# Kernel tuning notes

Hardware: AMD Instinct MI355X
Metric: run time of the kernel (lower is better)

## Reference

```python
import jax, jax.numpy as jnp
import numpy as np

B, T, HID = 2, 2048, 2048
H, DQ, DV, R = 16, 128, 128, 32
DCQ, DCKV, DCO = 768, 512, 512
EPS = 1e-6
SCALE = DQ ** -0.5


def _rms(x, w):
    xf = x.astype(jnp.float32)
    var = jnp.mean(xf * xf, axis=-1, keepdims=True)
    return w * (xf * jax.lax.rsqrt(var + EPS)).astype(x.dtype)


def _rotate_half(x):
    d = x.shape[-1] // 2
    return jnp.concatenate([-x[..., d:], x[..., :d]], axis=-1)


def setup_inputs() -> dict:
    key = jax.random.key(0)
    ks = jax.random.split(key, 9)
    s = 0.02
    hidden_states = jax.random.normal(ks[0], (B, T, HID), dtype=jnp.float32)
    # RoPE tables: inv_freq over R/2 dims, duplicated (cat(freqs, freqs))
    inv_freq = 1.0 / (10000.0 ** (np.arange(0, R, 2, dtype=np.float32) / R))
    freqs = np.arange(T, dtype=np.float32)[:, None] * inv_freq[None, :]  # [T, R/2]
    emb = np.concatenate([freqs, freqs], axis=-1)  # [T, R]
    cos = jnp.asarray(np.cos(emb))
    sin = jnp.asarray(np.sin(emb))
    return {
        "hidden_states": hidden_states,
        "cos": cos,
        "sin": sin,
        "Wq_shared": jax.random.normal(ks[1], (DCQ, HID), jnp.float32) * s,
        "q_shared_norm_w": jnp.ones((DCQ,), jnp.float32),
        "Wkv_shared": jax.random.normal(ks[2], (DCKV, HID), jnp.float32) * s,
        "kv_shared_norm_w": jnp.ones((DCKV,), jnp.float32),
        "Wq_private": jax.random.normal(ks[3], (H * DQ, DCQ), jnp.float32) * s,
        "Wkv_private": jax.random.normal(ks[4], (H * (DQ + DV), DCKV), jnp.float32) * s,
        "Wg_private": jax.random.normal(ks[5], (H * DV, HID), jnp.float32) * s,
        "Wo_private": jax.random.normal(ks[6], (DCO, H * DV), jnp.float32) * s,
        "o_private_norm_w": jnp.ones((DCO,), jnp.float32),
        "Wo_shared": jax.random.normal(ks[7], (HID, DCO), jnp.float32) * s,
    }


def reference(hidden_states, cos, sin, Wq_shared, q_shared_norm_w, Wkv_shared,
              kv_shared_norm_w, Wq_private, Wkv_private, Wg_private,
              Wo_private, o_private_norm_w, Wo_shared):
    x = hidden_states
    b, t, _ = x.shape
    # shared (latent) projections + RMSNorm
    q_shared = _rms(x @ Wq_shared.T, q_shared_norm_w)    # [B,T,DCQ]
    kv_shared = _rms(x @ Wkv_shared.T, kv_shared_norm_w)  # [B,T,DCKV]
    # private per-head projections
    q = (q_shared @ Wq_private.T).reshape(b, t, H, DQ).transpose(0, 2, 1, 3)
    kv = kv_shared @ Wkv_private.T                        # [B,T,H*(DQ+DV)]
    k_flat, v_flat = jnp.split(kv, 2, axis=-1)            # keys block then values block
    gates = jax.nn.silu(x @ Wg_private.T)                 # [B,T,H*DV]
    v_flat = v_flat * gates
    k = k_flat.reshape(b, t, H, DQ).transpose(0, 2, 1, 3)
    v = v_flat.reshape(b, t, H, DV).transpose(0, 2, 1, 3)
    # partial RoPE on first R dims of each head
    c = cos[None, None]  # [1,1,T,R]
    s = sin[None, None]
    q_rope, q_pass = q[..., :R], q[..., R:]
    k_rope, k_pass = k[..., :R], k[..., R:]
    q = jnp.concatenate([q_rope * c + _rotate_half(q_rope) * s, q_pass], axis=-1)
    k = jnp.concatenate([k_rope * c + _rotate_half(k_rope) * s, k_pass], axis=-1)
    # causal attention
    scores = jnp.einsum('bhqd,bhkd->bhqk', q, k) * SCALE
    causal = jnp.tril(jnp.ones((t, t), dtype=bool))
    scores = jnp.where(causal, scores, jnp.finfo(scores.dtype).min)
    attn = jax.nn.softmax(scores, axis=-1)
    out = jnp.einsum('bhqk,bhkd->bhqd', attn, v)
    out = out.transpose(0, 2, 1, 3).reshape(b, t, H * DV)
    # output subspace: private proj -> norm -> shared proj
    out = _rms(out @ Wo_private.T, o_private_norm_w)
    return out @ Wo_shared.T
```

## Files before the change

### kernel.cpp

```cpp
#include <hip/hip_runtime.h>
#include <stdint.h>

typedef __attribute__((ext_vector_type(8))) short short8;
typedef __attribute__((ext_vector_type(4))) short sh4;
typedef __attribute__((ext_vector_type(4))) float f32x4;

__device__ __forceinline__ float bf2f(unsigned short u) {
  union { unsigned int i; float f; } v; v.i = ((unsigned int)u) << 16; return v.f;
}
__device__ __forceinline__ unsigned short f2bf(float f) {
  union { float f; unsigned int i; } v; v.f = f;
  unsigned int u = v.i;
  return (unsigned short)((u + 0x7fffu + ((u >> 16) & 1u)) >> 16);
}

#define B_SZ 2
#define T_SEQ 2048
#define NH 16
#define DH 128
#define ROPE_R 32
#define SCALE_Q 0.08838834764831845f

template <bool F>
__device__ __forceinline__ short8 ld8(const void* base, size_t idx) {
  if constexpr (F) {
    const float* p = (const float*)base + idx;
    f32x4 a = *(const f32x4*)p;
    f32x4 b = *(const f32x4*)(p + 4);
    short8 r;
    r[0] = (short)f2bf(a[0]); r[1] = (short)f2bf(a[1]);
    r[2] = (short)f2bf(a[2]); r[3] = (short)f2bf(a[3]);
    r[4] = (short)f2bf(b[0]); r[5] = (short)f2bf(b[1]);
    r[6] = (short)f2bf(b[2]); r[7] = (short)f2bf(b[3]);
    return r;
  } else {
    return *(const short8*)((const unsigned short*)base + idx);
  }
}

template <bool AF, bool BF, bool C32>
__global__ __launch_bounds__(256) void gemm_bt(
    const void* __restrict__ Ap, const void* __restrict__ Bp,
    void* __restrict__ Cp, int M, int N, int K) {
  __shared__ unsigned short Al[128][40];
  __shared__ unsigned short Bl[128][40];
  const int tid = threadIdx.x;
  const int lane = tid & 63, w = tid >> 6;
  const int wm = w >> 1, wn = w & 1;
  const int quad = lane >> 4, l16 = lane & 15;
  const int m0 = blockIdx.y * 128, n0 = blockIdx.x * 128;
  f32x4 acc[4][4];
#pragma unroll
  for (int i = 0; i < 4; ++i)
#pragma unroll
    for (int j = 0; j < 4; ++j)
#pragma unroll
      for (int r = 0; r < 4; ++r) acc[i][j][r] = 0.f;

  for (int k0 = 0; k0 < K; k0 += 32) {
    __syncthreads();
#pragma unroll
    for (int p = 0; p < 2; ++p) {
      int v = tid + p * 256;
      int row = v >> 2, kc = (v & 3) * 8;
      *(short8*)&Al[row][kc] = ld8<AF>(Ap, (size_t)(m0 + row) * K + k0 + kc);
      *(short8*)&Bl[row][kc] = ld8<BF>(Bp, (size_t)(n0 + row) * K + k0 + kc);
    }
    __syncthreads();
    short8 a[4];
#pragma unroll
    for (int i = 0; i < 4; ++i)
      a[i] = *(const short8*)&Al[wm * 64 + i * 16 + l16][quad * 8];
#pragma unroll
    for (int j = 0; j < 4; ++j) {
      short8 b = *(const short8*)&Bl[wn * 64 + j * 16 + l16][quad * 8];
#pragma unroll
      for (int i = 0; i < 4; ++i)
        acc[i][j] = __builtin_amdgcn_mfma_f32_16x16x32_bf16(a[i], b, acc[i][j], 0, 0, 0);
    }
  }
#pragma unroll
  for (int i = 0; i < 4; ++i)
#pragma unroll
    for (int j = 0; j < 4; ++j) {
      int row = m0 + wm * 64 + i * 16 + quad * 4;
      int col = n0 + wn * 64 + j * 16 + l16;
#pragma unroll
      for (int r = 0; r < 4; ++r) {
        if constexpr (C32)
          ((float*)Cp)[(size_t)(row + r) * N + col] = acc[i][j][r];
        else
          ((unsigned short*)Cp)[(size_t)(row + r) * N + col] = f2bf(acc[i][j][r]);
      }
    }
}

__device__ __forceinline__ void gload_lds16(const unsigned short* g, unsigned short* l) {
  __builtin_amdgcn_global_load_lds(
      (const __attribute__((address_space(1))) void*)g,
      (__attribute__((address_space(3))) void*)l, 16, 0, 0);
}

template <int BN, bool C32>
__global__ __launch_bounds__(256) void gemm_lds(
    const unsigned short* __restrict__ A, const unsigned short* __restrict__ Bw,
    void* __restrict__ Cp, int M, int N, int K) {
  __shared__ unsigned short Al[128][32];
  __shared__ unsigned short Bl[BN][32];
  const int tid = threadIdx.x;
  const int lane = tid & 63, w = tid >> 6;
  const int wm = w >> 1, wn = w & 1;
  const int quad = lane >> 4, l16 = lane & 15;
  const int m0 = blockIdx.y * 128, n0 = blockIdx.x * BN;
  constexpr int NJ = BN / 32;
  f32x4 acc[4][NJ];
#pragma unroll
  for (int i = 0; i < 4; ++i)
#pragma unroll
    for (int j = 0; j < NJ; ++j)
#pragma unroll
      for (int r = 0; r < 4; ++r) acc[i][j][r] = 0.f;

  for (int k0 = 0; k0 < K; k0 += 32) {
    __syncthreads();
#pragma unroll
    for (int p = 0; p < 2; ++p) {
      int c = w * 128 + p * 64 + lane;
      gload_lds16(A + (size_t)(m0 + (c >> 2)) * K + k0 + (c & 3) * 8,
                  &Al[0][0] + (size_t)(w * 128 + p * 64) * 8);
    }
#pragma unroll
    for (int p = 0; p < BN / 64; ++p) {
      int c = w * BN + p * 64 + lane;
      gload_lds16(Bw + (size_t)(n0 + (c >> 2)) * K + k0 + (c & 3) * 8,
                  &Bl[0][0] + (size_t)(w * BN + p * 64) * 8);
    }
    __syncthreads();
    short8 a[4], b[NJ];
#pragma unroll
    for (int i = 0; i < 4; ++i)
      a[i] = *(const short8*)&Al[wm * 64 + i * 16 + l16][quad * 8];
#pragma unroll
    for (int j = 0; j < NJ; ++j)
      b[j] = *(const short8*)&Bl[wn * (BN / 2) + j * 16 + l16][quad * 8];
#pragma unroll
    for (int j = 0; j < NJ; ++j)
#pragma unroll
      for (int i = 0; i < 4; ++i)
        acc[i][j] = __builtin_amdgcn_mfma_f32_16x16x32_bf16(a[i], b[j], acc[i][j], 0, 0, 0);
  }
#pragma unroll
  for (int i = 0; i < 4; ++i)
#pragma unroll
    for (int j = 0; j < NJ; ++j) {
      int row = m0 + wm * 64 + i * 16 + quad * 4;
      int col = n0 + wn * (BN / 2) + j * 16 + l16;
#pragma unroll
      for (int r = 0; r < 4; ++r) {
        if constexpr (C32)
          ((float*)Cp)[(size_t)(row + r) * N + col] = acc[i][j][r];
        else
          ((unsigned short*)Cp)[(size_t)(row + r) * N + col] = f2bf(acc[i][j][r]);
      }
    }
}

struct CvtArgs {
  const float* src[8];
  unsigned short* dst[8];
  long long n4[8];
};

__global__ __launch_bounds__(256) void cvt_multi(CvtArgs a, long long total4) {
  for (long long g = (long long)blockIdx.x * 256 + threadIdx.x; g < total4;
       g += (long long)gridDim.x * 256) {
    long long r = g;
    int s = 0;
    while (r >= a.n4[s]) { r -= a.n4[s]; ++s; }
    f32x4 v = ((const f32x4*)a.src[s])[r];
    sh4 o;
    o[0] = (short)f2bf(v[0]); o[1] = (short)f2bf(v[1]);
    o[2] = (short)f2bf(v[2]); o[3] = (short)f2bf(v[3]);
    ((sh4*)a.dst[s])[r] = o;
  }
}

__global__ __launch_bounds__(256) void rms_norm_ip(
    unsigned short* __restrict__ x, const float* __restrict__ w, int N) {
  unsigned short* row = x + (size_t)blockIdx.x * N;
  float vals[8];
  int cnt = 0;
  float ss = 0.f;
  for (int j = threadIdx.x; j < N; j += 256) {
    float v = bf2f(row[j]);
    vals[cnt++] = v;
    ss += v * v;
  }
#pragma unroll
  for (int d = 1; d < 64; d <<= 1) ss += __shfl_xor(ss, d);
  __shared__ float ws4[4];
  if ((threadIdx.x & 63) == 0) ws4[threadIdx.x >> 6] = ss;
  __syncthreads();
  float tot = ws4[0] + ws4[1] + ws4[2] + ws4[3];
  float scale = rsqrtf(tot / (float)N + 1e-6f);
  cnt = 0;
  for (int j = threadIdx.x; j < N; j += 256)
    row[j] = f2bf(w[j] * vals[cnt++] * scale);
}

__global__ __launch_bounds__(256) void prep_qk(
    const unsigned short* __restrict__ q_all, const unsigned short* __restrict__ k_all,
    const float* __restrict__ cosb, const float* __restrict__ sinb,
    unsigned short* __restrict__ Q, unsigned short* __restrict__ K) {
  const int bt = blockIdx.x;
  const int b = bt >> 11, t = bt & (T_SEQ - 1);
  const unsigned short* qr = q_all + (size_t)bt * (NH * DH);
  const unsigned short* kr = k_all + (size_t)bt * (NH * DH);
  for (int d = threadIdx.x; d < NH * DH; d += 256) {
    int h = d >> 7, dd = d & 127;
    float qv = bf2f(qr[d]);
    float kv = bf2f(kr[d]);
    if (dd < ROPE_R) {
      float c = cosb[t * ROPE_R + dd];
      float s = sinb[t * ROPE_R + dd];
      float qrot = (dd < 16) ? -bf2f(qr[d + 16]) : bf2f(qr[d - 16]);
      float krot = (dd < 16) ? -bf2f(kr[d + 16]) : bf2f(kr[d - 16]);
      qv = qv * c + qrot * s;
      kv = kv * c + krot * s;
    }
    size_t o = ((size_t)(b * NH + h) * T_SEQ + t) * DH + dd;
    Q[o] = f2bf(qv * SCALE_Q);
    K[o] = f2bf(kv);
  }
}

__global__ __launch_bounds__(256) void prep_vt(
    const unsigned short* __restrict__ v_all, const unsigned short* __restrict__ gates,
    unsigned short* __restrict__ Vt) {
  __shared__ unsigned short tile[64][130];
  const int bh = blockIdx.y, b = bh >> 4, h = bh & 15;
  const int t0 = blockIdx.x * 64;
  for (int idx = threadIdx.x; idx < 64 * 128; idx += 256) {
    int tt = idx >> 7, dd = idx & 127;
    size_t rowbase = (size_t)(b * T_SEQ + t0 + tt);
    float v = bf2f(v_all[rowbase * (NH * DH) + h * DH + dd]);
    float g = bf2f(gates[rowbase * (NH * DH) + h * DH + dd]);
    float sg = g / (1.f + __expf(-g));
    tile[tt][dd] = f2bf(v * sg);
  }
  __syncthreads();
  for (int idx = threadIdx.x; idx < 64 * 128; idx += 256) {
    int dd = idx >> 6, tt = idx & 63;
    Vt[((size_t)bh * DH + dd) * T_SEQ + t0 + tt] = tile[tt][dd];
  }
}

__device__ __forceinline__ void attn_update(
    const unsigned short (*Kl)[132], const unsigned short (*Vl)[68],
    unsigned short (*Pw)[96], const short8* qf, int qt, int kb, bool diag,
    int wt, int quad, int l16, f32x4* O, float* m_run, float* l_part) {
  f32x4 sc[4];
  __builtin_amdgcn_s_setprio(1);
#pragma unroll
  for (int jt = 0; jt < 4; ++jt) {
#pragma unroll
    for (int r = 0; r < 4; ++r) sc[jt][r] = 0.f;
#pragma unroll
    for (int kk = 0; kk < 4; ++kk) {
      short8 kf = *(const short8*)&Kl[jt * 16 + l16][kk * 32 + quad * 8];
      sc[jt] = __builtin_amdgcn_mfma_f32_16x16x32_bf16(qf[kk], kf, sc[jt], 0, 0, 0);
    }
  }
  __builtin_amdgcn_s_setprio(0);
  if (diag) {
#pragma unroll
    for (int jt = 0; jt < 4; ++jt) {
      int key = kb + jt * 16 + l16;
#pragma unroll
      for (int r = 0; r < 4; ++r) {
        int row = qt * 64 + wt * 16 + quad * 4 + r;
        if (key > row) sc[jt][r] = -1e30f;
      }
    }
  }
  float pmax[4];
#pragma unroll
  for (int r = 0; r < 4; ++r)
    pmax[r] = fmaxf(fmaxf(sc[0][r], sc[1][r]), fmaxf(sc[2][r], sc[3][r]));
  bool near = (pmax[0] <= m_run[0] + 8.f) & (pmax[1] <= m_run[1] + 8.f) &
              (pmax[2] <= m_run[2] + 8.f) & (pmax[3] <= m_run[3] + 8.f);
  if (!__all((int)near)) {
    float alpha[4];
#pragma unroll
    for (int r = 0; r < 4; ++r) {
      float mx = pmax[r];
      mx = fmaxf(mx, __shfl_xor(mx, 1)); mx = fmaxf(mx, __shfl_xor(mx, 2));
      mx = fmaxf(mx, __shfl_xor(mx, 4)); mx = fmaxf(mx, __shfl_xor(mx, 8));
      float mnew = fmaxf(m_run[r], mx);
      alpha[r] = __expf(m_run[r] - mnew);
      m_run[r] = mnew;
    }
#pragma unroll
    for (int r = 0; r < 4; ++r) l_part[r] *= alpha[r];
#pragma unroll
    for (int jn = 0; jn < 8; ++jn)
#pragma unroll
      for (int r = 0; r < 4; ++r) O[jn][r] *= alpha[r];
  }
#pragma unroll
  for (int jt = 0; jt < 4; ++jt)
#pragma unroll
    for (int r = 0; r < 4; ++r) {
      float p = __expf(sc[jt][r] - m_run[r]);
      sc[jt][r] = p;
      l_part[r] += p;
    }
#pragma unroll
  for (int jt = 0; jt < 4; ++jt)
#pragma unroll
    for (int r = 0; r < 4; ++r)
      Pw[quad * 4 + r][jt * 16 + l16] = f2bf(sc[jt][r]);
  short8 pa[2];
#pragma unroll
  for (int kk = 0; kk < 2; ++kk)
    pa[kk] = *(const short8*)&Pw[l16][kk * 32 + quad * 8];
  __builtin_amdgcn_s_setprio(1);
#pragma unroll
  for (int jn = 0; jn < 8; ++jn) {
#pragma unroll
    for (int kk = 0; kk < 2; ++kk) {
      short8 vf = *(const short8*)&Vl[jn * 16 + l16][kk * 32 + quad * 8];
      O[jn] = __builtin_amdgcn_mfma_f32_16x16x32_bf16(pa[kk], vf, O[jn], 0, 0, 0);
    }
  }
  __builtin_amdgcn_s_setprio(0);
}

__global__ __launch_bounds__(512, 2) void flash_attn(
    const unsigned short* __restrict__ Q, const unsigned short* __restrict__ K,
    const unsigned short* __restrict__ Vt, unsigned short* __restrict__ Out) {
  __shared__ unsigned short Kl[64][132];
  __shared__ unsigned short Vl[128][68];
  __shared__ unsigned short P_lds[8][16][96];
  const int l = blockIdx.x;
  const int s = l & 7, qq = l >> 3;
  const int bh = s + 8 * (qq >> 4);
  const int qp = qq & 15;
  const int qa = qp, qb = 31 - qp;
  const int b = bh >> 4, h = bh & 15;
  const int tid = threadIdx.x;
  const int lane = tid & 63, w = tid >> 6;
  const int wt = w & 3;
  const bool isB = w >= 4;
  const int myq = isB ? qb : qa;
  const int quad = lane >> 4, l16 = lane & 15;
  const unsigned short* Qb = Q + (size_t)bh * T_SEQ * DH;
  const unsigned short* Kb = K + (size_t)bh * T_SEQ * DH;
  const unsigned short* Vb = Vt + (size_t)bh * DH * T_SEQ;

  short8 qf[4];
  const int qrow = myq * 64 + wt * 16 + l16;
#pragma unroll
  for (int kk = 0; kk < 4; ++kk)
    qf[kk] = *(const short8*)&Qb[(size_t)qrow * DH + kk * 32 + quad * 8];

  f32x4 O[8];
  float m_run[4], l_part[4];
#pragma unroll
  for (int jn = 0; jn < 8; ++jn)
#pragma unroll
    for (int r = 0; r < 4; ++r) O[jn][r] = 0.f;
#pragma unroll
  for (int r = 0; r < 4; ++r) { m_run[r] = -1e30f; l_part[r] = 0.f; }

  short8 krg[2], vrg[2];
#pragma unroll
  for (int p = 0; p < 2; ++p) {
    int id = tid + p * 512;
    krg[p] = *(const short8*)&Kb[(size_t)(id >> 4) * DH + (id & 15) * 8];
    vrg[p] = *(const short8*)&Vb[(size_t)(id >> 3) * T_SEQ + (id & 7) * 8];
  }
#pragma unroll
  for (int p = 0; p < 2; ++p) {
    int id = tid + p * 512;
    *(short8*)&Kl[id >> 4][(id & 15) * 8] = krg[p];
    *(short8*)&Vl[id >> 3][(id & 7) * 8] = vrg[p];
  }
  __syncthreads();

  const int last = qb;
  for (int kt = 0; kt <= last; ++kt) {
    const int kb = kt * 64;
    if (kt < last) {
      const int nb = kb + 64;
#pragma unroll
      for (int p = 0; p < 2; ++p) {
        int id = tid + p * 512;
        krg[p] = *(const short8*)&Kb[(size_t)(nb + (id >> 4)) * DH + (id & 15) * 8];
        vrg[p] = *(const short8*)&Vb[(size_t)(id >> 3) * T_SEQ + nb + (id & 7) * 8];
      }
    }
    if (isB || kt <= qa)
      attn_update(Kl, Vl, P_lds[w], qf, myq, kb, kt == (isB ? last : qa),
                  wt, quad, l16, O, m_run, l_part);
    if (kt < last) {
      __syncthreads();
#pragma unroll
      for (int p = 0; p < 2; ++p) {
        int id = tid + p * 512;
        *(short8*)&Kl[id >> 4][(id & 15) * 8] = krg[p];
        *(short8*)&Vl[id >> 3][(id & 7) * 8] = vrg[p];
      }
      __syncthreads();
    }
  }

  float l_run[4];
#pragma unroll
  for (int r = 0; r < 4; ++r) {
    float ssum = l_part[r];
    ssum += __shfl_xor(ssum, 1); ssum += __shfl_xor(ssum, 2);
    ssum += __shfl_xor(ssum, 4); ssum += __shfl_xor(ssum, 8);
    l_run[r] = ssum;
  }
#pragma unroll
  for (int jn = 0; jn < 8; ++jn)
#pragma unroll
    for (int r = 0; r < 4; ++r) {
      int rr = myq * 64 + wt * 16 + quad * 4 + r;
      Out[((size_t)(b * T_SEQ) + rr) * (NH * DH) + h * DH + jn * 16 + l16] =
          f2bf(O[jn][r] / l_run[r]);
    }
}

extern "C" void kernel_launch(void* const* d_in, const int* in_sizes, int n_in,
                              void* d_out, int out_size, void* d_ws, size_t ws_size,
                              hipStream_t stream) {
  const void*  x     = d_in[0];
  const float* cosb  = (const float*)d_in[1];
  const float* sinb  = (const float*)d_in[2];
  const void*  Wq_s  = d_in[3];
  const float* qs_w  = (const float*)d_in[4];
  const void*  Wkv_s = d_in[5];
  const float* kvs_w = (const float*)d_in[6];
  const void*  Wq_p  = d_in[7];
  const float* Wkv_p = (const float*)d_in[8];
  const void*  Wg_p  = d_in[9];
  const void*  Wo_p  = d_in[10];
  const float* o_w   = (const float*)d_in[11];
  const void*  Wo_s  = d_in[12];
  (void)in_sizes; (void)n_in; (void)out_size;

  const int M = B_SZ * T_SEQ;
  char* ws = (char*)d_ws;
  unsigned short* qs    = (unsigned short*)(ws + 0);
  unsigned short* omid  = qs;
  unsigned short* kvs   = (unsigned short*)(ws + 6291456);
  unsigned short* gates = (unsigned short*)(ws + 10485760);
  unsigned short* k_all = gates;
  unsigned short* v_all = (unsigned short*)(ws + 27262976);
  unsigned short* Qb    = v_all;
  unsigned short* Vt    = (unsigned short*)(ws + 44040192);
  unsigned short* Kb    = (unsigned short*)(ws + 60817408);
  unsigned short* q_all = (unsigned short*)d_out;
  unsigned short* attn  = (unsigned short*)d_out;

  dim3 blk(256);
  dim3 blk512(512);
  const size_t FAST_WS_NEEDED = 119537664;

  if (ws_size >= FAST_WS_NEEDED) {
    unsigned short* xb     = (unsigned short*)(ws + 77594624);
    unsigned short* Wq_s_b = (unsigned short*)(ws + 94371840);
    unsigned short* Wkv_s_b= (unsigned short*)(ws + 97517568);
    unsigned short* Wg_p_b = (unsigned short*)(ws + 99614720);
    unsigned short* Wq_p_b = (unsigned short*)(ws + 108003328);
    unsigned short* Wkv_p_b= (unsigned short*)(ws + 111149056);
    unsigned short* Wo_p_b = (unsigned short*)(ws + 115343360);
    unsigned short* Wo_s_b = (unsigned short*)(ws + 117440512);

    CvtArgs ca;
    ca.src[0] = (const float*)x;    ca.dst[0] = xb;      ca.n4[0] = 2097152;
    ca.src[1] = (const float*)Wq_s; ca.dst[1] = Wq_s_b;  ca.n4[1] = 393216;
    ca.src[2] = (const float*)Wkv_s;ca.dst[2] = Wkv_s_b; ca.n4[2] = 262144;
    ca.src[3] = (const float*)Wg_p; ca.dst[3] = Wg_p_b;  ca.n4[3] = 1048576;
    ca.src[4] = (const float*)Wq_p; ca.dst[4] = Wq_p_b;  ca.n4[4] = 393216;
    ca.src[5] = Wkv_p;              ca.dst[5] = Wkv_p_b; ca.n4[5] = 524288;
    ca.src[6] = (const float*)Wo_p; ca.dst[6] = Wo_p_b;  ca.n4[6] = 262144;
    ca.src[7] = (const float*)Wo_s; ca.dst[7] = Wo_s_b;  ca.n4[7] = 262144;
    long long total4 = 5242880;
    cvt_multi<<<dim3(2048), blk, 0, stream>>>(ca, total4);

    gemm_lds<128, false><<<dim3(768 / 128, M / 128), blk, 0, stream>>>(xb, Wq_s_b, qs, M, 768, 2048);
    gemm_lds<64,  false><<<dim3(512 / 64,  M / 128), blk, 0, stream>>>(xb, Wkv_s_b, kvs, M, 512, 2048);
    gemm_lds<128, false><<<dim3(2048 / 128, M / 128), blk, 0, stream>>>(xb, Wg_p_b, gates, M, 2048, 2048);
    rms_norm_ip<<<M, blk, 0, stream>>>(qs, qs_w, 768);
    rms_norm_ip<<<M, blk, 0, stream>>>(kvs, kvs_w, 512);
    gemm_lds<128, false><<<dim3(2048 / 128, M / 128), blk, 0, stream>>>(qs, Wq_p_b, q_all, M, 2048, 768);
    gemm_lds<128, false><<<dim3(2048 / 128, M / 128), blk, 0, stream>>>(
        kvs, Wkv_p_b + (size_t)2048 * 512, v_all, M, 2048, 512);
    prep_vt<<<dim3(T_SEQ / 64, B_SZ * NH), blk, 0, stream>>>(v_all, gates, Vt);
    gemm_lds<128, false><<<dim3(2048 / 128, M / 128), blk, 0, stream>>>(kvs, Wkv_p_b, k_all, M, 2048, 512);
    prep_qk<<<M, blk, 0, stream>>>(q_all, k_all, cosb, sinb, Qb, Kb);
    flash_attn<<<dim3(512), blk512, 0, stream>>>(Qb, Kb, Vt, attn);
    gemm_lds<64,  false><<<dim3(512 / 64, M / 128), blk, 0, stream>>>(attn, Wo_p_b, omid, M, 512, 2048);
    rms_norm_ip<<<M, blk, 0, stream>>>(omid, o_w, 512);
    gemm_lds<128, true><<<dim3(2048 / 128, M / 128), blk, 0, stream>>>(omid, Wo_s_b, d_out, M, 2048, 512);
  } else {
    gemm_bt<true, true, false><<<dim3(768 / 128, M / 128), blk, 0, stream>>>(x, Wq_s, qs, M, 768, 2048);
    gemm_bt<true, true, false><<<dim3(512 / 128, M / 128), blk, 0, stream>>>(x, Wkv_s, kvs, M, 512, 2048);
    gemm_bt<true, true, false><<<dim3(2048 / 128, M / 128), blk, 0, stream>>>(x, Wg_p, gates, M, 2048, 2048);
    rms_norm_ip<<<M, blk, 0, stream>>>(qs, qs_w, 768);
    rms_norm_ip<<<M, blk, 0, stream>>>(kvs, kvs_w, 512);
    gemm_bt<false, true, false><<<dim3(2048 / 128, M / 128), blk, 0, stream>>>(qs, Wq_p, q_all, M, 2048, 768);
    gemm_bt<false, true, false><<<dim3(2048 / 128, M / 128), blk, 0, stream>>>(
        kvs, Wkv_p + (size_t)2048 * 512, v_all, M, 2048, 512);
    prep_vt<<<dim3(T_SEQ / 64, B_SZ * NH), blk, 0, stream>>>(v_all, gates, Vt);
    gemm_bt<false, true, false><<<dim3(2048 / 128, M / 128), blk, 0, stream>>>(kvs, Wkv_p, k_all, M, 2048, 512);
    prep_qk<<<M, blk, 0, stream>>>(q_all, k_all, cosb, sinb, Qb, Kb);
    flash_attn<<<dim3(512), blk512, 0, stream>>>(Qb, Kb, Vt, attn);
    gemm_bt<false, true, false><<<dim3(512 / 128, M / 128), blk, 0, stream>>>(attn, Wo_p, omid, M, 512, 2048);
    rms_norm_ip<<<M, blk, 0, stream>>>(omid, o_w, 512);
    gemm_bt<false, true, true><<<dim3(2048 / 128, M / 128), blk, 0, stream>>>(omid, Wo_s, d_out, M, 2048, 512);
  }
}
```

Before: 699.8 us.

## Merge the three input-side projection GEMMs into one wide GEMM

The Wq_shared, Wkv_shared and Wg_private projections all read the same bf16 input. They are now computed by a single GEMM with N=3328, relying on the three converted weight buffers sitting back to back in the workspace. A leading-dimension argument is added to the GEMM, RMSNorm and V-prep kernels so later stages can read column slices of the merged output in place. This removes two launches and re-reads of the input and gives one larger, better-balanced grid. The cost is a strided output layout and workspace aliasing: K is written into the input buffer, and the merged buffer may overlap other regions.

```diff
diff --git a/kernel.cpp b/kernel.cpp
--- a/kernel.cpp
+++ b/kernel.cpp
@@ -104,7 +104,7 @@
 template <int BN, bool C32>
 __global__ __launch_bounds__(256) void gemm_lds(
     const unsigned short* __restrict__ A, const unsigned short* __restrict__ Bw,
-    void* __restrict__ Cp, int M, int N, int K) {
+    void* __restrict__ Cp, int M, int N, int K, int LDA) {
   __shared__ unsigned short Al[128][32];
   __shared__ unsigned short Bl[BN][32];
   const int tid = threadIdx.x;
@@ -126,7 +126,7 @@
 #pragma unroll
     for (int p = 0; p < 2; ++p) {
       int c = w * 128 + p * 64 + lane;
-      gload_lds16(A + (size_t)(m0 + (c >> 2)) * K + k0 + (c & 3) * 8,
+      gload_lds16(A + (size_t)(m0 + (c >> 2)) * LDA + k0 + (c & 3) * 8,
                   &Al[0][0] + (size_t)(w * 128 + p * 64) * 8);
     }
 #pragma unroll
@@ -186,8 +186,8 @@
 }
 
 __global__ __launch_bounds__(256) void rms_norm_ip(
-    unsigned short* __restrict__ x, const float* __restrict__ w, int N) {
-  unsigned short* row = x + (size_t)blockIdx.x * N;
+    unsigned short* __restrict__ x, const float* __restrict__ w, int N, int LD) {
+  unsigned short* row = x + (size_t)blockIdx.x * LD;
   float vals[8];
   int cnt = 0;
   float ss = 0.f;
@@ -236,7 +236,7 @@
 
 __global__ __launch_bounds__(256) void prep_vt(
     const unsigned short* __restrict__ v_all, const unsigned short* __restrict__ gates,
-    unsigned short* __restrict__ Vt) {
+    unsigned short* __restrict__ Vt, int gstride) {
   __shared__ unsigned short tile[64][130];
   const int bh = blockIdx.y, b = bh >> 4, h = bh & 15;
   const int t0 = blockIdx.x * 64;
@@ -244,7 +244,7 @@
     int tt = idx >> 7, dd = idx & 127;
     size_t rowbase = (size_t)(b * T_SEQ + t0 + tt);
     float v = bf2f(v_all[rowbase * (NH * DH) + h * DH + dd]);
-    float g = bf2f(gates[rowbase * (NH * DH) + h * DH + dd]);
+    float g = bf2f(gates[rowbase * (size_t)gstride + h * DH + dd]);
     float sg = g / (1.f + __expf(-g));
     tile[tt][dd] = f2bf(v * sg);
   }
@@ -478,6 +478,8 @@
     unsigned short* Wkv_p_b= (unsigned short*)(ws + 111149056);
     unsigned short* Wo_p_b = (unsigned short*)(ws + 115343360);
     unsigned short* Wo_s_b = (unsigned short*)(ws + 117440512);
+    unsigned short* merged = (unsigned short*)(ws + 0);
+    unsigned short* k_new  = xb;
 
     CvtArgs ca;
     ca.src[0] = (const float*)x;    ca.dst[0] = xb;      ca.n4[0] = 2097152;
@@ -491,36 +493,40 @@
     long long total4 = 5242880;
     cvt_multi<<<dim3(2048), blk, 0, stream>>>(ca, total4);
 
-    gemm_lds<128, false><<<dim3(768 / 128, M / 128), blk, 0, stream>>>(xb, Wq_s_b, qs, M, 768, 2048);
-    gemm_lds<64,  false><<<dim3(512 / 64,  M / 128), blk, 0, stream>>>(xb, Wkv_s_b, kvs, M, 512, 2048);
-    gemm_lds<128, false><<<dim3(2048 / 128, M / 128), blk, 0, stream>>>(xb, Wg_p_b, gates, M, 2048, 2048);
-    rms_norm_ip<<<M, blk, 0, stream>>>(qs, qs_w, 768);
-    rms_norm_ip<<<M, blk, 0, stream>>>(kvs, kvs_w, 512);
-    gemm_lds<128, false><<<dim3(2048 / 128, M / 128), blk, 0, stream>>>(qs, Wq_p_b, q_all, M, 2048, 768);
+    gemm_lds<128, false><<<dim3(3328 / 128, M / 128), blk, 0, stream>>>(
+        xb, Wq_s_b, merged, M, 3328, 2048, 2048);
+    rms_norm_ip<<<M, blk, 0, stream>>>(merged, qs_w, 768, 3328);
+    rms_norm_ip<<<M, blk, 0, stream>>>(merged + 768, kvs_w, 512, 3328);
     gemm_lds<128, false><<<dim3(2048 / 128, M / 128), blk, 0, stream>>>(
-        kvs, Wkv_p_b + (size_t)2048 * 512, v_all, M, 2048, 512);
-    prep_vt<<<dim3(T_SEQ / 64, B_SZ * NH), blk, 0, stream>>>(v_all, gates, Vt);
-    gemm_lds<128, false><<<dim3(2048 / 128, M / 128), blk, 0, stream>>>(kvs, Wkv_p_b, k_all, M, 2048, 512);
-    prep_qk<<<M, blk, 0, stream>>>(q_all, k_all, cosb, sinb, Qb, Kb);
+        merged, Wq_p_b, q_all, M, 2048, 768, 3328);
+    gemm_lds<128, false><<<dim3(2048 / 128, M / 128), blk, 0, stream>>>(
+        merged + 768, Wkv_p_b + (size_t)2048 * 512, v_all, M, 2048, 512, 3328);
+    prep_vt<<<dim3(T_SEQ / 64, B_SZ * NH), blk, 0, stream>>>(
+        v_all, merged + 1280, Vt, 3328);
+    gemm_lds<128, false><<<dim3(2048 / 128, M / 128), blk, 0, stream>>>(
+        merged + 768, Wkv_p_b, k_new, M, 2048, 512, 3328);
+    prep_qk<<<M, blk, 0, stream>>>(q_all, k_new, cosb, sinb, Qb, Kb);
     flash_attn<<<dim3(512), blk512, 0, stream>>>(Qb, Kb, Vt, attn);
-    gemm_lds<64,  false><<<dim3(512 / 64, M / 128), blk, 0, stream>>>(attn, Wo_p_b, omid, M, 512, 2048);
-    rms_norm_ip<<<M, blk, 0, stream>>>(omid, o_w, 512);
-    gemm_lds<128, true><<<dim3(2048 / 128, M / 128), blk, 0, stream>>>(omid, Wo_s_b, d_out, M, 2048, 512);
+    gemm_lds<64, false><<<dim3(512 / 64, M / 128), blk, 0, stream>>>(
+        attn, Wo_p_b, omid, M, 512, 2048, 2048);
+    rms_norm_ip<<<M, blk, 0, stream>>>(omid, o_w, 512, 512);
+    gemm_lds<128, true><<<dim3(2048 / 128, M / 128), blk, 0, stream>>>(
+        omid, Wo_s_b, d_out, M, 2048, 512, 512);
   } else {
     gemm_bt<true, true, false><<<dim3(768 / 128, M / 128), blk, 0, stream>>>(x, Wq_s, qs, M, 768, 2048);
     gemm_bt<true, true, false><<<dim3(512 / 128, M / 128), blk, 0, stream>>>(x, Wkv_s, kvs, M, 512, 2048);
     gemm_bt<true, true, false><<<dim3(2048 / 128, M / 128), blk, 0, stream>>>(x, Wg_p, gates, M, 2048, 2048);
-    rms_norm_ip<<<M, blk, 0, stream>>>(qs, qs_w, 768);
-    rms_norm_ip<<<M, blk, 0, stream>>>(kvs, kvs_w, 512);
+    rms_norm_ip<<<M, blk, 0, stream>>>(qs, qs_w, 768, 768);
+    rms_norm_ip<<<M, blk, 0, stream>>>(kvs, kvs_w, 512, 512);
     gemm_bt<false, true, false><<<dim3(2048 / 128, M / 128), blk, 0, stream>>>(qs, Wq_p, q_all, M, 2048, 768);
     gemm_bt<false, true, false><<<dim3(2048 / 128, M / 128), blk, 0, stream>>>(
         kvs, Wkv_p + (size_t)2048 * 512, v_all, M, 2048, 512);
-    prep_vt<<<dim3(T_SEQ / 64, B_SZ * NH), blk, 0, stream>>>(v_all, gates, Vt);
+    prep_vt<<<dim3(T_SEQ / 64, B_SZ * NH), blk, 0, stream>>>(v_all, gates, Vt, 2048);
     gemm_bt<false, true, false><<<dim3(2048 / 128, M / 128), blk, 0, stream>>>(kvs, Wkv_p, k_all, M, 2048, 512);
     prep_qk<<<M, blk, 0, stream>>>(q_all, k_all, cosb, sinb, Qb, Kb);
     flash_attn<<<dim3(512), blk512, 0, stream>>>(Qb, Kb, Vt, attn);
     gemm_bt<false, true, false><<<dim3(512 / 128, M / 128), blk, 0, stream>>>(attn, Wo_p, omid, M, 512, 2048);
-    rms_norm_ip<<<M, blk, 0, stream>>>(omid, o_w, 512);
+    rms_norm_ip<<<M, blk, 0, stream>>>(omid, o_w, 512, 512);
     gemm_bt<false, true, true><<<dim3(2048 / 128, M / 128), blk, 0, stream>>>(omid, Wo_s, d_out, M, 2048, 512);
   }
 }
```

Result: faster. 668.4 us (-4.5%).
